# Performance work log

Hardware: AMD Instinct MI355X
Metric: run time of the kernel (lower is better)

Reference implementation:

```python
import jax, jax.numpy as jnp
import numpy as np

N_NODES = 100000
N_EDGES = 3200000
D_IN = 128
D_OUT = 128


def setup_inputs() -> dict:
    key = jax.random.key(0)
    k1, k2, k3, k4, k5, k6 = jax.random.split(key, 6)
    x = jax.random.normal(k1, (N_NODES, D_IN), dtype=jnp.float32)
    edge_row = jnp.sort(jax.random.randint(k2, (N_EDGES,), 0, N_NODES, dtype=jnp.int32))
    edge_col = jax.random.randint(k3, (N_EDGES,), 0, N_NODES, dtype=jnp.int32)
    edge_val = jax.random.uniform(k4, (N_EDGES,), dtype=jnp.float32)
    stdv = 1.0 / np.sqrt(D_OUT)
    weight = jax.random.uniform(k5, (D_IN, D_OUT), dtype=jnp.float32, minval=-stdv, maxval=stdv)
    bias = jax.random.uniform(k6, (D_OUT,), dtype=jnp.float32, minval=-stdv, maxval=stdv)
    return {"x": x, "edge_row": edge_row, "edge_col": edge_col,
            "edge_val": edge_val, "weight": weight, "bias": bias}


def reference(x, edge_row, edge_col, edge_val, weight, bias):
    # support = A @ x  (sparse COO SpMM via gather + segment-sum scatter)
    gathered = x[edge_col] * edge_val[:, None]          # [E, D_IN]
    support = jax.ops.segment_sum(gathered, edge_row, num_segments=N_NODES)  # [N, D_IN]
    # output = support @ W + b
    return support @ weight + bias
```

## Files before the change

### kernel.cpp

```cpp
#include <hip/hip_runtime.h>

#define NNODES 100000
#define NEDGES 3200000
#define DIM    128

typedef __bf16  bf16x8 __attribute__((ext_vector_type(8)));
typedef unsigned short u16;
typedef u16     u16x8  __attribute__((ext_vector_type(8)));
typedef float   f32x4  __attribute__((ext_vector_type(4)));
typedef unsigned int u32;
typedef u32     u32x2  __attribute__((ext_vector_type(2)));

__device__ __forceinline__ u16 f2bf(float f) {
    union { float f; unsigned int i; } c;
    c.f = f;
    unsigned int x = c.i;
    unsigned int rounding = 0x7fff + ((x >> 16) & 1);
    x += rounding;
    return (u16)(x >> 16);
}

__device__ __forceinline__ float bf2f(u16 u) {
    union { unsigned int i; float f; } c;
    c.i = ((unsigned int)u) << 16;
    return c.f;
}

__device__ __forceinline__ bf16x8 ldfrag_u16(const u16* p) {
    u16x8 u = *(const u16x8*)p;
    return __builtin_bit_cast(bf16x8, u);
}

__device__ __forceinline__ bf16x8 ldfrag_f32(const float* p) {
    f32x4 a = *(const f32x4*)p;
    f32x4 b = *(const f32x4*)(p + 4);
    u16x8 u;
#pragma unroll
    for (int i = 0; i < 4; ++i) u[i] = f2bf(a[i]);
#pragma unroll
    for (int i = 0; i < 4; ++i) u[4 + i] = f2bf(b[i]);
    return __builtin_bit_cast(bf16x8, u);
}

__global__ void build_row_ptr(const int* __restrict__ edge_row,
                              int* __restrict__ row_ptr) {
    int n = blockIdx.x * blockDim.x + threadIdx.x;
    if (n > NNODES) return;
    int lo = 0, hi = NEDGES;
    while (lo < hi) {
        int mid = (lo + hi) >> 1;
        if (edge_row[mid] < n) lo = mid + 1; else hi = mid;
    }
    row_ptr[n] = lo;
}

__global__ void prep_wt(const float* __restrict__ w, u16* __restrict__ wt) {
    int i = blockIdx.x * blockDim.x + threadIdx.x;
    if (i >= DIM * DIM) return;
    int k = i >> 7, n = i & 127;
    wt[n * DIM + k] = f2bf(w[k * DIM + n]);
}

#define WT_STRIDE 136
__global__ __launch_bounds__(256) void gemm_xw(const float* __restrict__ x,
                                               const u16* __restrict__ wt,
                                               u16* __restrict__ y) {
    __shared__ u16 wlds[DIM * WT_STRIDE];

    int tid = threadIdx.x;
    {
        const f32x4* src = (const f32x4*)wt;
#pragma unroll
        for (int i = 0; i < 8; ++i) {
            int ci  = tid + 256 * i;
            int row = ci >> 4, off = ci & 15;
            *((f32x4*)(wlds + row * WT_STRIDE) + off) = src[ci];
        }
    }
    __syncthreads();

    int wave = __builtin_amdgcn_readfirstlane(tid >> 6);
    int lane = tid & 63;
    int quad = lane >> 4, l16 = lane & 15;
    int mBase = (blockIdx.x * 4 + wave) * 16;
    if (mBase >= NNODES) return;

    const float* xrow = x + (size_t)(mBase + l16) * DIM + quad * 8;

    f32x4 acc[8];
#pragma unroll
    for (int nt = 0; nt < 8; ++nt) acc[nt] = (f32x4){0.f, 0.f, 0.f, 0.f};

#pragma unroll
    for (int kb = 0; kb < 4; ++kb) {
        bf16x8 a = ldfrag_f32(xrow + kb * 32);
#pragma unroll
        for (int nt = 0; nt < 8; ++nt) {
            bf16x8 b = ldfrag_u16(wlds + (nt * 16 + l16) * WT_STRIDE + kb * 32 + quad * 8);
            acc[nt] = __builtin_amdgcn_mfma_f32_16x16x32_bf16(a, b, acc[nt], 0, 0, 0);
        }
    }

#pragma unroll
    for (int nt = 0; nt < 8; ++nt) {
        int col = nt * 16 + l16;
#pragma unroll
        for (int r = 0; r < 4; ++r) {
            int row = mBase + quad * 4 + r;
            y[(size_t)row * DIM + col] = f2bf(acc[nt][r]);
        }
    }
}

__global__ __launch_bounds__(256) void spmm(const int* __restrict__ row_ptr,
                                            const int* __restrict__ ecol,
                                            const float* __restrict__ eval,
                                            const u16* __restrict__ y,
                                            const float* __restrict__ bias,
                                            float* __restrict__ out) {
    int wave = threadIdx.x >> 6;
    int lane = threadIdx.x & 63;
    int half = lane >> 5;
    int l32  = lane & 31;
    int row  = blockIdx.x * 4 + wave;
    if (row >= NNODES) return;

    int lo = row_ptr[row];
    int hi = row_ptr[row + 1];

    float a0 = 0.f, a1 = 0.f, a2 = 0.f, a3 = 0.f;
    const u16* yb = y + l32 * 4;

    int e = lo;
    for (; e + 8 <= hi; e += 8) {
        int c[4]; float v[4];
#pragma unroll
        for (int s = 0; s < 4; ++s) {
            c[s] = __builtin_nontemporal_load(ecol + e + 2 * s + half);
            v[s] = __builtin_nontemporal_load(eval + e + 2 * s + half);
        }
        u32x2 p[4];
#pragma unroll
        for (int s = 0; s < 4; ++s)
            p[s] = *(const u32x2*)(yb + (size_t)c[s] * DIM);
#pragma unroll
        for (int s = 0; s < 4; ++s) {
            a0 += v[s] * bf2f((u16)(p[s][0] & 0xffffu));
            a1 += v[s] * bf2f((u16)(p[s][0] >> 16));
            a2 += v[s] * bf2f((u16)(p[s][1] & 0xffffu));
            a3 += v[s] * bf2f((u16)(p[s][1] >> 16));
        }
    }
    for (; e + 2 <= hi; e += 2) {
        int   c = __builtin_nontemporal_load(ecol + e + half);
        float v = __builtin_nontemporal_load(eval + e + half);
        u32x2 p = *(const u32x2*)(yb + (size_t)c * DIM);
        a0 += v * bf2f((u16)(p[0] & 0xffffu));
        a1 += v * bf2f((u16)(p[0] >> 16));
        a2 += v * bf2f((u16)(p[1] & 0xffffu));
        a3 += v * bf2f((u16)(p[1] >> 16));
    }
    if (e < hi && half == 0) {
        int   c = ecol[e];
        float v = eval[e];
        u32x2 p = *(const u32x2*)(yb + (size_t)c * DIM);
        a0 += v * bf2f((u16)(p[0] & 0xffffu));
        a1 += v * bf2f((u16)(p[0] >> 16));
        a2 += v * bf2f((u16)(p[1] & 0xffffu));
        a3 += v * bf2f((u16)(p[1] >> 16));
    }

    a0 += __shfl_xor(a0, 32);
    a1 += __shfl_xor(a1, 32);
    a2 += __shfl_xor(a2, 32);
    a3 += __shfl_xor(a3, 32);

    if (half == 0) {
        f32x4 o;
        o[0] = a0 + bias[l32 * 4 + 0];
        o[1] = a1 + bias[l32 * 4 + 1];
        o[2] = a2 + bias[l32 * 4 + 2];
        o[3] = a3 + bias[l32 * 4 + 3];
        __builtin_nontemporal_store(o, (f32x4*)(out + (size_t)row * DIM + l32 * 4));
    }
}

extern "C" void kernel_launch(void* const* d_in, const int* in_sizes, int n_in,
                              void* d_out, int out_size, void* d_ws, size_t ws_size,
                              hipStream_t stream) {
    const float* x        = (const float*)d_in[0];
    const int*   edge_row = (const int*)d_in[1];
    const int*   edge_col = (const int*)d_in[2];
    const float* edge_val = (const float*)d_in[3];
    const float* weight   = (const float*)d_in[4];
    const float* bias     = (const float*)d_in[5];
    float* out = (float*)d_out;

    char* ws = (char*)d_ws;
    u16* y       = (u16*)ws;
    int* row_ptr = (int*)(ws + (size_t)NNODES * DIM * 2);
    u16* wt      = (u16*)(ws + 26000128);

    prep_wt<<<(DIM * DIM + 255) / 256, 256, 0, stream>>>(weight, wt);
    build_row_ptr<<<(NNODES + 1 + 255) / 256, 256, 0, stream>>>(edge_row, row_ptr);

    gemm_xw<<<(NNODES / 16 + 3) / 4, 256, 0, stream>>>(x, wt, y);

    spmm<<<NNODES / 4, 256, 0, stream>>>(row_ptr, edge_col, edge_val, y, bias, out);
}
```

Before: 276.6 us.

## Bounce GEMM output through LDS for coalesced stores; remap SpMM lanes to full rows

In the x@W GEMM, each wave now writes its 16x128 bf16 tile into a per-wave LDS buffer and then stores it to global memory as 16-byte vectors, replacing scattered 2-byte stores. In the SpMM, each wave now covers a whole output row with 64 lanes of 2 columns, instead of two half-waves that each split the edges and reduce with a shuffle. Edge indices and values become wave-uniform scalar loads, so the cross-lane reduction goes away. The bf16 unpacking now uses a shift or mask, and each gather fetch shrinks to 4 bytes per lane, which may mean more load instructions for the same bytes moved.

```diff
diff --git a/kernel.cpp b/kernel.cpp
--- a/kernel.cpp
+++ b/kernel.cpp
@@ -8,8 +8,8 @@
 typedef unsigned short u16;
 typedef u16     u16x8  __attribute__((ext_vector_type(8)));
 typedef float   f32x4  __attribute__((ext_vector_type(4)));
+typedef float   f32x2  __attribute__((ext_vector_type(2)));
 typedef unsigned int u32;
-typedef u32     u32x2  __attribute__((ext_vector_type(2)));
 
 __device__ __forceinline__ u16 f2bf(float f) {
     union { float f; unsigned int i; } c;
@@ -20,10 +20,8 @@
     return (u16)(x >> 16);
 }
 
-__device__ __forceinline__ float bf2f(u16 u) {
-    union { unsigned int i; float f; } c;
-    c.i = ((unsigned int)u) << 16;
-    return c.f;
+__device__ __forceinline__ float asf(u32 u) {
+    union { u32 i; float f; } c; c.i = u; return c.f;
 }
 
 __device__ __forceinline__ bf16x8 ldfrag_u16(const u16* p) {
@@ -66,6 +64,7 @@
                                                const u16* __restrict__ wt,
                                                u16* __restrict__ y) {
     __shared__ u16 wlds[DIM * WT_STRIDE];
+    __shared__ u16 ybounce[4][16 * DIM];
 
     int tid = threadIdx.x;
     {
@@ -101,14 +100,19 @@
         }
     }
 
+    u16* yb = ybounce[wave];
 #pragma unroll
     for (int nt = 0; nt < 8; ++nt) {
         int col = nt * 16 + l16;
 #pragma unroll
-        for (int r = 0; r < 4; ++r) {
-            int row = mBase + quad * 4 + r;
-            y[(size_t)row * DIM + col] = f2bf(acc[nt][r]);
-        }
+        for (int r = 0; r < 4; ++r)
+            yb[(quad * 4 + r) * DIM + col] = f2bf(acc[nt][r]);
+    }
+#pragma unroll
+    for (int j = 0; j < 4; ++j) {
+        int lr = j * 4 + quad;
+        u16x8 t = *(const u16x8*)(yb + lr * DIM + l16 * 8);
+        *(u16x8*)(y + (size_t)(mBase + lr) * DIM + l16 * 8) = t;
     }
 }
 
@@ -118,71 +122,55 @@
                                             const u16* __restrict__ y,
                                             const float* __restrict__ bias,
                                             float* __restrict__ out) {
-    int wave = threadIdx.x >> 6;
     int lane = threadIdx.x & 63;
-    int half = lane >> 5;
-    int l32  = lane & 31;
-    int row  = blockIdx.x * 4 + wave;
+    int row  = __builtin_amdgcn_readfirstlane(blockIdx.x * 4 + (threadIdx.x >> 6));
     if (row >= NNODES) return;
 
     int lo = row_ptr[row];
     int hi = row_ptr[row + 1];
 
-    float a0 = 0.f, a1 = 0.f, a2 = 0.f, a3 = 0.f;
-    const u16* yb = y + l32 * 4;
+    const u16* yl = y + lane * 2;
+    float acc0 = 0.f, acc1 = 0.f;
 
     int e = lo;
     for (; e + 8 <= hi; e += 8) {
+        int c[8]; float v[8];
+#pragma unroll
+        for (int s = 0; s < 8; ++s) { c[s] = ecol[e + s]; v[s] = eval[e + s]; }
+        u32 p[8];
+#pragma unroll
+        for (int s = 0; s < 8; ++s) p[s] = *(const u32*)(yl + (size_t)c[s] * DIM);
+#pragma unroll
+        for (int s = 0; s < 8; ++s) {
+            acc0 += v[s] * asf(p[s] << 16);
+            acc1 += v[s] * asf(p[s] & 0xffff0000u);
+        }
+    }
+    for (; e + 4 <= hi; e += 4) {
         int c[4]; float v[4];
 #pragma unroll
-        for (int s = 0; s < 4; ++s) {
-            c[s] = __builtin_nontemporal_load(ecol + e + 2 * s + half);
-            v[s] = __builtin_nontemporal_load(eval + e + 2 * s + half);
-        }
-        u32x2 p[4];
+        for (int s = 0; s < 4; ++s) { c[s] = ecol[e + s]; v[s] = eval[e + s]; }
+        u32 p[4];
 #pragma unroll
-        for (int s = 0; s < 4; ++s)
-            p[s] = *(const u32x2*)(yb + (size_t)c[s] * DIM);
+        for (int s = 0; s < 4; ++s) p[s] = *(const u32*)(yl + (size_t)c[s] * DIM);
 #pragma unroll
         for (int s = 0; s < 4; ++s) {
-            a0 += v[s] * bf2f((u16)(p[s][0] & 0xffffu));
-            a1 += v[s] * bf2f((u16)(p[s][0] >> 16));
-            a2 += v[s] * bf2f((u16)(p[s][1] & 0xffffu));
-            a3 += v[s] * bf2f((u16)(p[s][1] >> 16));
+            acc0 += v[s] * asf(p[s] << 16);
+            acc1 += v[s] * asf(p[s] & 0xffff0000u);
         }
     }
-    for (; e + 2 <= hi; e += 2) {
-        int   c = __builtin_nontemporal_load(ecol + e + half);
-        float v = __builtin_nontemporal_load(eval + e + half);
-        u32x2 p = *(const u32x2*)(yb + (size_t)c * DIM);
-        a0 += v * bf2f((u16)(p[0] & 0xffffu));
-        a1 += v * bf2f((u16)(p[0] >> 16));
-        a2 += v * bf2f((u16)(p[1] & 0xffffu));
-        a3 += v * bf2f((u16)(p[1] >> 16));
-    }
-    if (e < hi && half == 0) {
+    for (; e < hi; ++e) {
         int   c = ecol[e];
         float v = eval[e];
-        u32x2 p = *(const u32x2*)(yb + (size_t)c * DIM);
-        a0 += v * bf2f((u16)(p[0] & 0xffffu));
-        a1 += v * bf2f((u16)(p[0] >> 16));
-        a2 += v * bf2f((u16)(p[1] & 0xffffu));
-        a3 += v * bf2f((u16)(p[1] >> 16));
+        u32   p = *(const u32*)(yl + (size_t)c * DIM);
+        acc0 += v * asf(p << 16);
+        acc1 += v * asf(p & 0xffff0000u);
     }
 
-    a0 += __shfl_xor(a0, 32);
-    a1 += __shfl_xor(a1, 32);
-    a2 += __shfl_xor(a2, 32);
-    a3 += __shfl_xor(a3, 32);
-
-    if (half == 0) {
-        f32x4 o;
-        o[0] = a0 + bias[l32 * 4 + 0];
-        o[1] = a1 + bias[l32 * 4 + 1];
-        o[2] = a2 + bias[l32 * 4 + 2];
-        o[3] = a3 + bias[l32 * 4 + 3];
-        __builtin_nontemporal_store(o, (f32x4*)(out + (size_t)row * DIM + l32 * 4));
-    }
+    f32x2 o;
+    o[0] = acc0 + bias[lane * 2];
+    o[1] = acc1 + bias[lane * 2 + 1];
+    __builtin_nontemporal_store(o, (f32x2*)(out + (size_t)row * DIM + lane * 2));
 }
 
 extern "C" void kernel_launch(void* const* d_in, const int* in_sizes, int n_in,
```

Measured after the change: 248.8 us. -10.1%, faster.
